# Kernel tuning notes

Measured on AMD Instinct MI355X. Metric: run time of the kernel, lower is better.

## Reference

```python
import jax, jax.numpy as jnp
import numpy as np

B, CLEN, QLEN, H = 32, 384, 64, 768


def _p(key, shape, scale=0.02):
    return jax.random.normal(key, shape, dtype=jnp.float32) * scale


def setup_inputs() -> dict:
    key = jax.random.key(0)
    ks = iter(jax.random.split(key, 64))
    d = {}
    d["c"] = jax.random.normal(next(ks), (B, CLEN, H), jnp.float32)
    d["q"] = jax.random.normal(next(ks), (B, QLEN, H), jnp.float32)
    d["w_att_c"] = _p(next(ks), (H,)); d["b_att_c"] = jnp.zeros((), jnp.float32)
    d["w_att_q"] = _p(next(ks), (H,)); d["b_att_q"] = jnp.zeros((), jnp.float32)
    d["w_att_cq"] = _p(next(ks), (H,)); d["b_att_cq"] = jnp.zeros((), jnp.float32)
    def add_lstm(prefix, in_dim):
        for dr in ("f", "b"):
            d[prefix + dr + "_wih"] = _p(next(ks), (4 * H, in_dim))
            d[prefix + dr + "_whh"] = _p(next(ks), (4 * H, H))
            d[prefix + dr + "_b"] = jnp.zeros((4 * H,), jnp.float32)  # b_ih + b_hh fused
    add_lstm("l1", 4 * H)  # modeling_LSTM1: input 4H
    add_lstm("l2", 2 * H)  # modeling_LSTM2: input 2H
    add_lstm("lo", 2 * H)  # output_LSTM: input 2H
    d["p1_wg"] = _p(next(ks), (4 * H,)); d["p1_bg"] = jnp.zeros((), jnp.float32)
    d["p1_wm"] = _p(next(ks), (2 * H,)); d["p1_bm"] = jnp.zeros((), jnp.float32)
    d["p2_wg"] = _p(next(ks), (4 * H,)); d["p2_bg"] = jnp.zeros((), jnp.float32)
    d["p2_wm"] = _p(next(ks), (2 * H,)); d["p2_bm"] = jnp.zeros((), jnp.float32)
    return d


def _lstm_dir(x, wih, whh, b):
    # single-direction LSTM, torch gate order (i, f, g, o)
    Bb, T, _ = x.shape
    Hh = whh.shape[1]
    xg = jnp.einsum("bti,gi->btg", x, wih) + b  # precompute input projections [B,T,4H]
    def step(carry, xt):
        h, cst = carry
        g = xt + h @ whh.T
        i, f, gg, o = jnp.split(g, 4, axis=-1)
        i = jax.nn.sigmoid(i); f = jax.nn.sigmoid(f)
        gg = jnp.tanh(gg); o = jax.nn.sigmoid(o)
        cst = f * cst + i * gg
        h = o * jnp.tanh(cst)
        return (h, cst), h
    init = (jnp.zeros((Bb, Hh), x.dtype), jnp.zeros((Bb, Hh), x.dtype))
    _, hs = jax.lax.scan(step, init, jnp.swapaxes(xg, 0, 1))
    return jnp.swapaxes(hs, 0, 1)


def _bilstm(x, fwih, fwhh, fb, bwih, bwhh, bb):
    hf = _lstm_dir(x, fwih, fwhh, fb)
    hb = _lstm_dir(x[:, ::-1], bwih, bwhh, bb)[:, ::-1]
    return jnp.concatenate([hf, hb], axis=-1)


def _forward(c, q,
             w_att_c, b_att_c, w_att_q, b_att_q, w_att_cq, b_att_cq,
             l1f_wih, l1f_whh, l1f_b, l1b_wih, l1b_whh, l1b_b,
             l2f_wih, l2f_whh, l2f_b, l2b_wih, l2b_whh, l2b_b,
             lof_wih, lof_whh, lof_b, lob_wih, lob_whh, lob_b,
             p1_wg, p1_bg, p1_wm, p1_bm, p2_wg, p2_bg, p2_wm, p2_bm):
    # --- att_flow_layer: trilinear similarity collapsed to a single einsum ---
    # original loops over q_len applying att_weight_cq(c * q_i); equivalent to:
    cq = jnp.einsum("bih,bjh,h->bij", c, q, w_att_cq) + b_att_cq  # [B,C,Q]
    s = (c @ w_att_c + b_att_c)[:, :, None] + (q @ w_att_q + b_att_q)[:, None, :] + cq
    a = jax.nn.softmax(s, axis=2)                       # attend context->query
    c2q = jnp.einsum("bij,bjh->bih", a, q)              # [B,C,H]
    b_w = jax.nn.softmax(jnp.max(s, axis=2), axis=1)    # [B,C]
    q2c = jnp.einsum("bi,bih->bh", b_w, c)[:, None, :]  # [B,1,H]
    g = jnp.concatenate([c, c2q, c * c2q, c * q2c], axis=-1)  # [B,C,8H? no, 4H]

    # --- modeling layers (two stacked biLSTMs) ---
    m1 = _bilstm(g, l1f_wih, l1f_whh, l1f_b, l1b_wih, l1b_whh, l1b_b)
    m = _bilstm(m1, l2f_wih, l2f_whh, l2f_b, l2b_wih, l2b_whh, l2b_b)

    # --- output layer ---
    p1 = (g @ p1_wg + p1_bg) + (m @ p1_wm + p1_bm)      # [B,C]
    m2 = _bilstm(m, lof_wih, lof_whh, lof_b, lob_wih, lob_whh, lob_b)
    p2 = (g @ p2_wg + p2_bg) + (m2 @ p2_wm + p2_bm)
    return p1, p2


def reference(c, q,
              w_att_c, b_att_c, w_att_q, b_att_q, w_att_cq, b_att_cq,
              l1f_wih, l1f_whh, l1f_b, l1b_wih, l1b_whh, l1b_b,
              l2f_wih, l2f_whh, l2f_b, l2b_wih, l2b_whh, l2b_b,
              lof_wih, lof_whh, lof_b, lob_wih, lob_whh, lob_b,
              p1_wg, p1_bg, p1_wm, p1_bm, p2_wg, p2_bg, p2_wm, p2_bm):
    return _forward(c, q,
                    w_att_c, b_att_c, w_att_q, b_att_q, w_att_cq, b_att_cq,
                    l1f_wih, l1f_whh, l1f_b, l1b_wih, l1b_whh, l1b_b,
                    l2f_wih, l2f_whh, l2f_b, l2b_wih, l2b_whh, l2b_b,
                    lof_wih, lof_whh, lof_b, lob_wih, lob_whh, lob_b,
                    p1_wg, p1_bg, p1_wm, p1_bm, p2_wg, p2_bg, p2_wm, p2_bm)
```

## Files before the change

### kernel.cpp

```cpp
#include <hip/hip_runtime.h>


typedef __bf16 bf16_t;
typedef __bf16 bf16x4 __attribute__((ext_vector_type(4)));
typedef __bf16 bf16x8 __attribute__((ext_vector_type(8)));
typedef float  f32x4  __attribute__((ext_vector_type(4)));
typedef unsigned long long ull;

#define TT 384

__device__ __forceinline__ void gload_lds16(const void* g, void* l) {
  __builtin_amdgcn_global_load_lds((const __attribute__((address_space(1))) void*)g,
                                   (__attribute__((address_space(3))) void*)l, 16, 0, 0);
}

__global__ void k_zeroE(unsigned* p) {
  int i = blockIdx.x * 256 + threadIdx.x;
  __hip_atomic_store(p + i, 0xFFFF0000u, __ATOMIC_RELAXED, __HIP_MEMORY_SCOPE_AGENT);
}

template<int BN, int EPI, int BSRC>
__global__ __launch_bounds__(256) void k_gemm(
    const bf16_t* __restrict__ A, const void* __restrict__ Bv, const void* __restrict__ Bv2,
    int nsplit, void* __restrict__ Cv,
    int M, int N, int K, long sAb, long sBb, long sCb,
    const float* __restrict__ rowb, const float* __restrict__ colb,
    const float* __restrict__ sb)
{
  constexpr int BM = 128, BK = 32;
  constexpr int NT = BN / 32;
  __shared__ bf16_t sA[BM * BK];
  __shared__ bf16_t sB[BN * BK];
  const int t    = threadIdx.x;
  const int lane = t & 63;
  const int wm   = (t >> 6) >> 1, wn = (t >> 6) & 1;
  const long bz  = blockIdx.z;
  const int nbase = blockIdx.y * BN;
  const bf16_t* Ab = A + bz * sAb + (long)blockIdx.x * BM * K;
  const bf16_t* Bb = nullptr;
  const float*  Bf = nullptr;
  if constexpr (BSRC == 0)
    Bb = (const bf16_t*)Bv + bz * sBb + (long)nbase * K;
  else
    Bf = (nbase < nsplit) ? ((const float*)Bv  + (long)nbase * K)
                          : ((const float*)Bv2 + (long)(nbase - nsplit) * K);

  const int r4 = t >> 2;
  const int kq = (t & 3) ^ ((r4 >> 1) & 3);

  f32x4 acc[4][NT];
  #pragma unroll
  for (int i = 0; i < 4; i++)
    #pragma unroll
    for (int j = 0; j < NT; j++) acc[i][j] = (f32x4){0.f, 0.f, 0.f, 0.f};

  const int mrow = lane & 15;
  const int fq   = lane >> 4;
  const int aswz = (fq ^ ((mrow >> 1) & 3)) * 8;

  for (int k0 = 0; k0 < K; k0 += BK) {
    __syncthreads();
    gload_lds16(Ab + (long)r4 * K + k0 + kq * 8,        (char*)sA + t * 16);
    gload_lds16(Ab + (long)(64 + r4) * K + k0 + kq * 8, (char*)sA + 4096 + t * 16);
    if constexpr (BSRC == 0) {
      gload_lds16(Bb + (long)r4 * K + k0 + kq * 8,        (char*)sB + t * 16);
      if constexpr (BN == 128)
        gload_lds16(Bb + (long)(64 + r4) * K + k0 + kq * 8, (char*)sB + 4096 + t * 16);
    } else {
      {
        f32x4 b0 = *(const f32x4*)(Bf + (long)r4 * K + k0 + kq * 8);
        f32x4 b1 = *(const f32x4*)(Bf + (long)r4 * K + k0 + kq * 8 + 4);
        bf16x8 bb;
        #pragma unroll
        for (int e = 0; e < 4; e++) { bb[e] = (bf16_t)b0[e]; bb[e + 4] = (bf16_t)b1[e]; }
        *(bf16x8*)((char*)sB + t * 16) = bb;
      }
      if constexpr (BN == 128) {
        f32x4 b0 = *(const f32x4*)(Bf + (long)(64 + r4) * K + k0 + kq * 8);
        f32x4 b1 = *(const f32x4*)(Bf + (long)(64 + r4) * K + k0 + kq * 8 + 4);
        bf16x8 bb;
        #pragma unroll
        for (int e = 0; e < 4; e++) { bb[e] = (bf16_t)b0[e]; bb[e + 4] = (bf16_t)b1[e]; }
        *(bf16x8*)((char*)sB + 4096 + t * 16) = bb;
      }
    }
    __syncthreads();

    bf16x8 af[4], bv[NT];
    #pragma unroll
    for (int mt = 0; mt < 4; mt++)
      af[mt] = *(const bf16x8*)(sA + (wm * 64 + mt * 16 + mrow) * 32 + aswz);
    #pragma unroll
    for (int nt = 0; nt < NT; nt++)
      bv[nt] = *(const bf16x8*)(sB + (wn * (BN / 2) + nt * 16 + mrow) * 32 + aswz);
    #pragma unroll
    for (int mt = 0; mt < 4; mt++)
      #pragma unroll
      for (int nt = 0; nt < NT; nt++)
        acc[mt][nt] = __builtin_amdgcn_mfma_f32_16x16x32_bf16(af[mt], bv[nt], acc[mt][nt], 0, 0, 0);
  }

  const int rbase = (lane >> 4) * 4;
  #pragma unroll
  for (int mt = 0; mt < 4; mt++)
    #pragma unroll
    for (int nt = 0; nt < NT; nt++)
      #pragma unroll
      for (int r = 0; r < 4; r++) {
        int grow = blockIdx.x * BM + wm * 64 + mt * 16 + rbase + r;
        int gcol = nbase + wn * (BN / 2) + nt * 16 + (lane & 15);
        if constexpr (EPI == 0) {
          ((bf16_t*)Cv)[bz * sCb + (long)grow * N + gcol] = (bf16_t)acc[mt][nt][r];
        } else {
          ((float*)Cv)[bz * sCb + (long)grow * N + gcol] =
              acc[mt][nt][r] + rowb[bz * M + grow] + colb[bz * N + gcol] + sb[0];
        }
      }
}

__global__ __launch_bounds__(256) void k_lstm(
    const bf16_t* __restrict__ xg, bf16_t* __restrict__ mout,
    unsigned* __restrict__ E,
    const float* __restrict__ whh_f, const float* __restrict__ whh_b,
    const float* __restrict__ bias_f, const float* __restrict__ bias_b,
    int tagbase)
{
  __shared__ bf16_t sW[64 * 776];
  __shared__ bf16_t sH[16 * 776];
  __shared__ float  sG[4 * 256];
  const int t    = threadIdx.x;
  const int lane = t & 63;
  const int wg   = t >> 6;
  const int blk  = blockIdx.x;
  const int dir  = blk / 96;
  const int qq   = blk - dir * 96;
  const int sl   = qq >> 1;
  const int bg   = qq & 1;
  const int j0   = sl * 16;
  const float* whh  = dir ? whh_b : whh_f;
  const float* bias = dir ? bias_b : bias_f;

  for (int r = 0; r < 64; r++) {
    if (t < 192) {
      const float* src = whh + (long)((r >> 4) * 768 + j0 + (r & 15)) * 768 + t * 4;
      f32x4 v = *(const f32x4*)src;
      bf16x4 o; o[0] = (bf16_t)v[0]; o[1] = (bf16_t)v[1]; o[2] = (bf16_t)v[2]; o[3] = (bf16_t)v[3];
      *(bf16x4*)(sW + r * 776 + t * 4) = o;
    }
  }
  const int b16 = t >> 4;
  const int jj  = t & 15;
  float bsv[4];
  #pragma unroll
  for (int gi = 0; gi < 4; gi++) bsv[gi] = bias[gi * 768 + j0 + jj];

  int soff[24];
  #pragma unroll
  for (int i = 0; i < 24; i++) {
    int e = i * 256 + t;
    soff[i] = (e / 384) * 1552 + (e % 384) * 4;
  }

  float cst = 0.f;
  const int mrow  = lane & 15;
  const int fq    = lane >> 4;
  const int boff  = (wg * 16 + mrow) * 776 + fq * 8;
  const int aoff0 = mrow * 776 + fq * 8;
  const long xrow0 = (long)(bg * 16 + b16) * TT;

  for (int s = 0; s < TT; s++) {
    const int tc = dir ? (TT - 1 - s) : s;

    float xv[4];
    {
      long xr = (xrow0 + tc) * 6144 + dir * 3072 + j0 + jj;
      #pragma unroll
      for (int gi = 0; gi < 4; gi++) xv[gi] = (float)xg[xr + gi * 768];
    }

    if (s == 0) {
      for (int e = t; e < 1552; e += 256)
        *(f32x4*)((char*)sH + e * 16) = (f32x4){0.f, 0.f, 0.f, 0.f};
    } else {
      const unsigned want = (unsigned)(tagbase + s - 1);
      const int par = (s - 1) & 1;
      const ull* src = (const ull*)E + ((long)(par * 2 + dir) * 32 + bg * 16) * 384;
      ull qv[24];
      #pragma unroll
      for (int i = 0; i < 24; i++)
        qv[i] = __hip_atomic_load(src + i * 256 + t, __ATOMIC_RELAXED, __HIP_MEMORY_SCOPE_AGENT);
      for (;;) {
        unsigned bad = 0;
        #pragma unroll
        for (int i = 0; i < 24; i++) {
          unsigned lo = (unsigned)qv[i], hi = (unsigned)(qv[i] >> 32);
          if ((lo >> 16) != want || (hi >> 16) != want) bad |= 1u << i;
        }
        if (!bad) break;
        #pragma unroll
        for (int i = 0; i < 24; i++)
          if (bad & (1u << i))
            qv[i] = __hip_atomic_load(src + i * 256 + t, __ATOMIC_RELAXED, __HIP_MEMORY_SCOPE_AGENT);
      }
      #pragma unroll
      for (int i = 0; i < 24; i++) {
        ushort2 hh;
        hh.x = (unsigned short)qv[i];
        hh.y = (unsigned short)(qv[i] >> 32);
        *(ushort2*)((char*)sH + soff[i]) = hh;
      }
    }
    __syncthreads();

    f32x4 a0 = (f32x4){0.f, 0.f, 0.f, 0.f};
    #pragma unroll
    for (int kc = 0; kc < 24; kc++) {
      bf16x8 bv = *(const bf16x8*)(sW + boff + kc * 32);
      bf16x8 av = *(const bf16x8*)(sH + aoff0 + kc * 32);
      a0 = __builtin_amdgcn_mfma_f32_16x16x32_bf16(av, bv, a0, 0, 0, 0);
    }
    #pragma unroll
    for (int r = 0; r < 4; r++)
      sG[wg * 256 + (fq * 4 + r) * 16 + mrow] = a0[r];
    __syncthreads();

    {
      float gi = sG[0 * 256 + t] + xv[0] + bsv[0];
      float gf = sG[1 * 256 + t] + xv[1] + bsv[1];
      float gg = sG[2 * 256 + t] + xv[2] + bsv[2];
      float go = sG[3 * 256 + t] + xv[3] + bsv[3];
      gi = 1.f / (1.f + __expf(-gi));
      gf = 1.f / (1.f + __expf(-gf));
      gg = 1.f - 2.f / (__expf(2.f * gg) + 1.f);
      go = 1.f / (1.f + __expf(-go));
      cst = gf * cst + gi * gg;
      float hv = go * (1.f - 2.f / (__expf(2.f * cst) + 1.f));
      union { bf16_t b; unsigned short u; } pk;
      pk.b = (bf16_t)hv;
      unsigned tag = (unsigned)(tagbase + s);
      long ed = ((long)((s & 1) * 2 + dir) * 32 + bg * 16 + b16) * 768 + j0 + jj;
      __hip_atomic_store(E + ed, (tag << 16) | pk.u,
                         __ATOMIC_RELAXED, __HIP_MEMORY_SCOPE_AGENT);
      mout[(xrow0 + tc) * 1536 + dir * 768 + j0 + jj] = pk.b;
    }
  }
}


__global__ __launch_bounds__(256) void k_pack(
    const float* __restrict__ c, const float* __restrict__ q,
    const float* __restrict__ wcq, bf16_t* __restrict__ cw, bf16_t* __restrict__ qb)
{
  int i = blockIdx.x * 256 + threadIdx.x;
  if (i < 9437184) {
    int h = i % 768;
    cw[i] = (bf16_t)(c[i] * wcq[h]);
  } else {
    int j = i - 9437184;
    qb[j] = (bf16_t)q[j];
  }
}

__global__ __launch_bounds__(256) void k_proj(
    const float* __restrict__ c, const float* __restrict__ q,
    const float* __restrict__ wc, const float* __restrict__ bc,
    const float* __restrict__ wq, const float* __restrict__ bq,
    float* __restrict__ projc, float* __restrict__ projq)
{
  int row  = blockIdx.x * 4 + (threadIdx.x >> 6);
  int lane = threadIdx.x & 63;
  const float *src, *w;
  bool isC = row < 12288;
  if (isC) { src = c + (long)row * 768;          w = wc; }
  else     { src = q + (long)(row - 12288) * 768; w = wq; }
  float a = 0.f;
  for (int k = lane * 4; k < 768; k += 256) {
    f32x4 v = *(const f32x4*)(src + k);
    f32x4 wv = *(const f32x4*)(w + k);
    a += v[0]*wv[0] + v[1]*wv[1] + v[2]*wv[2] + v[3]*wv[3];
  }
  for (int m = 32; m; m >>= 1) a += __shfl_xor(a, m);
  if (lane == 0) {
    if (isC) projc[row] = a + bc[0];
    else     projq[row - 12288] = a + bq[0];
  }
}

__global__ __launch_bounds__(256) void k_smax_j(
    const float* __restrict__ s, bf16_t* __restrict__ a, float* __restrict__ smax)
{
  int row  = blockIdx.x * 4 + (threadIdx.x >> 6);
  int lane = threadIdx.x & 63;
  float v = s[(long)row * 64 + lane];
  float mx = v;
  for (int m = 32; m; m >>= 1) mx = fmaxf(mx, __shfl_xor(mx, m));
  float p = __expf(v - mx);
  float sum = p;
  for (int m = 32; m; m >>= 1) sum += __shfl_xor(sum, m);
  a[(long)row * 64 + lane] = (bf16_t)(p / sum);
  if (lane == 0) smax[row] = mx;
}

__global__ __launch_bounds__(384) void k_smax_i(
    const float* __restrict__ smax, float* __restrict__ bw)
{
  __shared__ float red[8];
  int b = blockIdx.x, t = threadIdx.x;
  int lane = t & 63, wv = t >> 6;
  float v = smax[b * 384 + t];
  float mx = v;
  for (int m = 32; m; m >>= 1) mx = fmaxf(mx, __shfl_xor(mx, m));
  if (lane == 0) red[wv] = mx;
  __syncthreads();
  float gm = red[0];
  #pragma unroll
  for (int i = 1; i < 6; i++) gm = fmaxf(gm, red[i]);
  float p = __expf(v - gm);
  float sm = p;
  for (int m = 32; m; m >>= 1) sm += __shfl_xor(sm, m);
  __syncthreads();
  if (lane == 0) red[wv] = sm;
  __syncthreads();
  float tot = red[0];
  #pragma unroll
  for (int i = 1; i < 6; i++) tot += red[i];
  bw[b * 384 + t] = p / tot;
}

__global__ __launch_bounds__(256) void k_q2c(
    const float* __restrict__ bw, const float* __restrict__ c, float* __restrict__ q2c)
{
  int b = blockIdx.y;
  int h = blockIdx.x * 256 + threadIdx.x;
  const float* cb = c + (long)b * 384 * 768;
  float acc = 0.f;
  for (int i = 0; i < 384; i++) acc += bw[b * 384 + i] * cb[(long)i * 768 + h];
  q2c[b * 768 + h] = acc;
}

__global__ __launch_bounds__(256) void k_tq(
    const bf16_t* __restrict__ qb, bf16_t* __restrict__ qT)
{
  __shared__ bf16_t sT[64][72];
  int b = blockIdx.y, hc = blockIdx.x, t = threadIdx.x;
  {
    int j = t >> 2, h0 = (t & 3) * 16;
    const bf16_t* src = qb + (long)(b * 64 + j) * 768 + hc * 64 + h0;
    *(bf16x8*)&sT[j][h0]     = *(const bf16x8*)(src);
    *(bf16x8*)&sT[j][h0 + 8] = *(const bf16x8*)(src + 8);
  }
  __syncthreads();
  {
    int h = t >> 2, j0 = (t & 3) * 16;
    bf16x8 o0, o1;
    #pragma unroll
    for (int e = 0; e < 8; e++) { o0[e] = sT[j0 + e][h]; o1[e] = sT[j0 + 8 + e][h]; }
    bf16_t* dst = qT + (long)(b * 768 + hc * 64 + h) * 64 + j0;
    *(bf16x8*)dst       = o0;
    *(bf16x8*)(dst + 8) = o1;
  }
}

__global__ __launch_bounds__(256) void k_buildg(
    const float* __restrict__ c, const bf16_t* __restrict__ c2q,
    const float* __restrict__ q2c, bf16_t* __restrict__ g)
{
  int i = blockIdx.x * 256 + threadIdx.x;
  int h = i % 768;
  int row = i / 768;
  int b = row / 384;
  float cv  = c[i];
  float cqv = (float)c2q[i];
  float qcv = q2c[b * 768 + h];
  bf16_t* gr = g + (long)row * 3072;
  gr[h]        = (bf16_t)cv;
  gr[768 + h]  = c2q[i];
  gr[1536 + h] = (bf16_t)(cv * cqv);
  gr[2304 + h] = (bf16_t)(cv * qcv);
}

__global__ __launch_bounds__(256) void k_headsg(
    const bf16_t* __restrict__ g, const float* __restrict__ w1, const float* __restrict__ w2,
    float* __restrict__ pg1, float* __restrict__ pg2)
{
  int row  = blockIdx.x * 4 + (threadIdx.x >> 6);
  int lane = threadIdx.x & 63;
  float a1 = 0.f, a2 = 0.f;
  const bf16_t* gr = g + (long)row * 3072;
  for (int k = lane * 8; k < 3072; k += 512) {
    bf16x8 v = *(const bf16x8*)(gr + k);
    f32x4 wa = *(const f32x4*)(w1 + k), wb = *(const f32x4*)(w1 + k + 4);
    f32x4 xa = *(const f32x4*)(w2 + k), xb = *(const f32x4*)(w2 + k + 4);
    #pragma unroll
    for (int e = 0; e < 4; e++) {
      a1 += (float)v[e] * wa[e] + (float)v[e + 4] * wb[e];
      a2 += (float)v[e] * xa[e] + (float)v[e + 4] * xb[e];
    }
  }
  for (int m_ = 32; m_; m_ >>= 1) { a1 += __shfl_xor(a1, m_); a2 += __shfl_xor(a2, m_); }
  if (lane == 0) { pg1[row] = a1; pg2[row] = a2; }
}

__global__ __launch_bounds__(256) void k_headsm(
    const bf16_t* __restrict__ m, const float* __restrict__ wm,
    const float* __restrict__ pg, const float* __restrict__ bg,
    const float* __restrict__ bm, float* __restrict__ out)
{
  int row  = blockIdx.x * 4 + (threadIdx.x >> 6);
  int lane = threadIdx.x & 63;
  float a = 0.f;
  const bf16_t* mr = m + (long)row * 1536;
  for (int k = lane * 8; k < 1536; k += 512) {
    bf16x8 v = *(const bf16x8*)(mr + k);
    f32x4 wa = *(const f32x4*)(wm + k), wb = *(const f32x4*)(wm + k + 4);
    #pragma unroll
    for (int e = 0; e < 4; e++) a += (float)v[e] * wa[e] + (float)v[e + 4] * wb[e];
  }
  for (int m_ = 32; m_; m_ >>= 1) a += __shfl_xor(a, m_);
  if (lane == 0) out[row] = pg[row] + a + bg[0] + bm[0];
}


extern "C" void kernel_launch(void* const* d_in, const int* in_sizes, int n_in,
                              void* d_out, int out_size, void* d_ws, size_t ws_size,
                              hipStream_t stream)
{
  (void)in_sizes; (void)n_in; (void)out_size; (void)ws_size;
  const float* c    = (const float*)d_in[0];
  const float* q    = (const float*)d_in[1];
  const float* wac  = (const float*)d_in[2];
  const float* bac  = (const float*)d_in[3];
  const float* waq  = (const float*)d_in[4];
  const float* baq  = (const float*)d_in[5];
  const float* wacq = (const float*)d_in[6];
  const float* bacq = (const float*)d_in[7];
  const float* l1f_wih = (const float*)d_in[8];
  const float* l1f_whh = (const float*)d_in[9];
  const float* l1f_b   = (const float*)d_in[10];
  const float* l1b_wih = (const float*)d_in[11];
  const float* l1b_whh = (const float*)d_in[12];
  const float* l1b_b   = (const float*)d_in[13];
  const float* l2f_wih = (const float*)d_in[14];
  const float* l2f_whh = (const float*)d_in[15];
  const float* l2f_b   = (const float*)d_in[16];
  const float* l2b_wih = (const float*)d_in[17];
  const float* l2b_whh = (const float*)d_in[18];
  const float* l2b_b   = (const float*)d_in[19];
  const float* lof_wih = (const float*)d_in[20];
  const float* lof_whh = (const float*)d_in[21];
  const float* lof_b   = (const float*)d_in[22];
  const float* lob_wih = (const float*)d_in[23];
  const float* lob_whh = (const float*)d_in[24];
  const float* lob_b   = (const float*)d_in[25];
  const float* p1wg = (const float*)d_in[26];
  const float* p1bg = (const float*)d_in[27];
  const float* p1wm = (const float*)d_in[28];
  const float* p1bm = (const float*)d_in[29];
  const float* p2wg = (const float*)d_in[30];
  const float* p2bg = (const float*)d_in[31];
  const float* p2wm = (const float*)d_in[32];
  const float* p2bm = (const float*)d_in[33];

  char* ws = (char*)d_ws;
  bf16_t* g_bf = (bf16_t*)ws;
  bf16_t* mA   = (bf16_t*)ws;
  bf16_t* mB   = (bf16_t*)(ws + 37748736L);
  bf16_t* m2   = (bf16_t*)ws;
  char*   xgc  = ws + 75497472L;
  bf16_t* xg   = (bf16_t*)xgc;
  bf16_t* cw  = (bf16_t*)xgc;
  bf16_t* qb  = (bf16_t*)(xgc + 18874368L);
  bf16_t* qT  = (bf16_t*)(xgc + 22020096L);
  float*  sS  = (float*) (xgc + 25165824L);
  bf16_t* aP  = (bf16_t*)(xgc + 28311552L);
  bf16_t* c2q = (bf16_t*)(xgc + 29884416L);
  char* tail = ws + 226492416L;
  float*    projc = (float*)tail;
  float*    projq = (float*)(tail + 49152);
  float*    smax  = (float*)(tail + 57344);
  float*    bw    = (float*)(tail + 106496);
  float*    q2c   = (float*)(tail + 155648);
  float*    pg1   = (float*)(tail + 253952);
  float*    pg2   = (float*)(tail + 303104);
  unsigned* E     = (unsigned*)(tail + 352256);

  k_zeroE<<<768, 256, 0, stream>>>(E);

  k_pack<<<43008, 256, 0, stream>>>(c, q, wacq, cw, qb);
  k_proj<<<3584, 256, 0, stream>>>(c, q, wac, bac, waq, baq, projc, projq);
  k_gemm<64,1,0><<<dim3(3,1,32), 256, 0, stream>>>(cw, qb, nullptr, 1<<30, sS,
      384, 64, 768, (long)384*768, (long)64*768, (long)384*64, projc, projq, bacq);
  k_smax_j<<<3072, 256, 0, stream>>>(sS, aP, smax);
  k_smax_i<<<32, 384, 0, stream>>>(smax, bw);
  k_q2c<<<dim3(3,32), 256, 0, stream>>>(bw, c, q2c);
  k_tq<<<dim3(12,32), 256, 0, stream>>>(qb, qT);
  k_gemm<64,0,0><<<dim3(3,12,32), 256, 0, stream>>>(aP, qT, nullptr, 1<<30, c2q,
      384, 768, 64, (long)384*64, (long)768*64, (long)384*768, nullptr, nullptr, nullptr);
  k_buildg<<<36864, 256, 0, stream>>>(c, c2q, q2c, g_bf);
  k_headsg<<<3072, 256, 0, stream>>>(g_bf, p1wg, p2wg, pg1, pg2);

  k_gemm<128,0,1><<<dim3(96,48,1), 256, 0, stream>>>(g_bf, l1f_wih, l1b_wih, 3072, xg,
      12288, 6144, 3072, 0, 0, 0, nullptr, nullptr, nullptr);
  k_lstm<<<192, 256, 0, stream>>>(xg, mA, E, l1f_whh, l1b_whh, l1f_b, l1b_b, 0);

  k_gemm<128,0,1><<<dim3(96,48,1), 256, 0, stream>>>(mA, l2f_wih, l2b_wih, 3072, xg,
      12288, 6144, 1536, 0, 0, 0, nullptr, nullptr, nullptr);
  k_lstm<<<192, 256, 0, stream>>>(xg, mB, E, l2f_whh, l2b_whh, l2f_b, l2b_b, 384);
  k_headsm<<<3072, 256, 0, stream>>>(mB, p1wm, pg1, p1bg, p1bm, (float*)d_out);

  k_gemm<128,0,1><<<dim3(96,48,1), 256, 0, stream>>>(mB, lof_wih, lob_wih, 3072, xg,
      12288, 6144, 1536, 0, 0, 0, nullptr, nullptr, nullptr);
  k_lstm<<<192, 256, 0, stream>>>(xg, m2, E, lof_whh, lob_whh, lof_b, lob_b, 768);
  k_headsm<<<3072, 256, 0, stream>>>(m2, p2wm, pg2, p2bg, p2bm, (float*)d_out + 12288);
}
```

Measured before the change: 6.965 ms.

## Hold recurrent LSTM weights in registers, halve block count with 512-thread blocks

The persistent LSTM kernel now keeps each wave's slice of W_hh in VGPRs as bf16 fragments instead of in LDS, and each block covers 32 hidden units with 8 waves instead of 16 units with 4 waves. The grid drops from 192 to 96 blocks, so fewer blocks take part in the per-step global flag synchronisation and each block polls half as much of the exchange buffer per thread. The MFMA loop is split into two independent accumulators, and the gate scratch in LDS is padded to avoid bank conflicts. In exchange, each block does twice the matrix work per step with fewer CUs active, and 24 bf16x8 weight registers per thread increase register pressure.

Result: faster. 6.563 ms (-5.8%).

```diff
diff --git a/kernel.cpp b/kernel.cpp
--- a/kernel.cpp
+++ b/kernel.cpp
@@ -118,53 +118,60 @@
       }
 }
 
-__global__ __launch_bounds__(256) void k_lstm(
+__global__ __launch_bounds__(512) void k_lstm(
     const bf16_t* __restrict__ xg, bf16_t* __restrict__ mout,
     unsigned* __restrict__ E,
     const float* __restrict__ whh_f, const float* __restrict__ whh_b,
     const float* __restrict__ bias_f, const float* __restrict__ bias_b,
     int tagbase)
 {
-  __shared__ bf16_t sW[64 * 776];
   __shared__ bf16_t sH[16 * 776];
-  __shared__ float  sG[4 * 256];
+  __shared__ float  sG[4 * 544];
   const int t    = threadIdx.x;
   const int lane = t & 63;
-  const int wg   = t >> 6;
+  const int w    = t >> 6;
+  const int g    = w & 3;
+  const int ch   = w >> 2;
   const int blk  = blockIdx.x;
-  const int dir  = blk / 96;
-  const int qq   = blk - dir * 96;
+  const int dir  = blk / 48;
+  const int qq   = blk - dir * 48;
   const int sl   = qq >> 1;
   const int bg   = qq & 1;
-  const int j0   = sl * 16;
+  const int j0   = sl * 32;
   const float* whh  = dir ? whh_b : whh_f;
   const float* bias = dir ? bias_b : bias_f;
 
-  for (int r = 0; r < 64; r++) {
-    if (t < 192) {
-      const float* src = whh + (long)((r >> 4) * 768 + j0 + (r & 15)) * 768 + t * 4;
-      f32x4 v = *(const f32x4*)src;
-      bf16x4 o; o[0] = (bf16_t)v[0]; o[1] = (bf16_t)v[1]; o[2] = (bf16_t)v[2]; o[3] = (bf16_t)v[3];
-      *(bf16x4*)(sW + r * 776 + t * 4) = o;
-    }
-  }
-  const int b16 = t >> 4;
-  const int jj  = t & 15;
+  const int mrow = lane & 15;
+  const int fq   = lane >> 4;
+
+  bf16x8 bw[24];
+  {
+    const float* wrow = whh + (long)(g * 768 + j0 + ch * 16 + mrow) * 768 + fq * 8;
+    #pragma unroll
+    for (int kc = 0; kc < 24; kc++) {
+      f32x4 v0 = *(const f32x4*)(wrow + kc * 32);
+      f32x4 v1 = *(const f32x4*)(wrow + kc * 32 + 4);
+      bf16x8 bb;
+      #pragma unroll
+      for (int e = 0; e < 4; e++) { bb[e] = (bf16_t)v0[e]; bb[e + 4] = (bf16_t)v1[e]; }
+      bw[kc] = bb;
+    }
+  }
+
+  const int b16 = t >> 5;
+  const int jj  = t & 31;
   float bsv[4];
   #pragma unroll
   for (int gi = 0; gi < 4; gi++) bsv[gi] = bias[gi * 768 + j0 + jj];
 
-  int soff[24];
+  int soff[12];
   #pragma unroll
-  for (int i = 0; i < 24; i++) {
-    int e = i * 256 + t;
+  for (int i = 0; i < 12; i++) {
+    int e = i * 512 + t;
     soff[i] = (e / 384) * 1552 + (e % 384) * 4;
   }
 
   float cst = 0.f;
-  const int mrow  = lane & 15;
-  const int fq    = lane >> 4;
-  const int boff  = (wg * 16 + mrow) * 776 + fq * 8;
   const int aoff0 = mrow * 776 + fq * 8;
   const long xrow0 = (long)(bg * 16 + b16) * TT;
 
@@ -179,31 +186,31 @@
     }
 
     if (s == 0) {
-      for (int e = t; e < 1552; e += 256)
+      for (int e = t; e < 1552; e += 512)
         *(f32x4*)((char*)sH + e * 16) = (f32x4){0.f, 0.f, 0.f, 0.f};
     } else {
       const unsigned want = (unsigned)(tagbase + s - 1);
       const int par = (s - 1) & 1;
       const ull* src = (const ull*)E + ((long)(par * 2 + dir) * 32 + bg * 16) * 384;
-      ull qv[24];
+      ull qv[12];
       #pragma unroll
-      for (int i = 0; i < 24; i++)
-        qv[i] = __hip_atomic_load(src + i * 256 + t, __ATOMIC_RELAXED, __HIP_MEMORY_SCOPE_AGENT);
+      for (int i = 0; i < 12; i++)
+        qv[i] = __hip_atomic_load(src + i * 512 + t, __ATOMIC_RELAXED, __HIP_MEMORY_SCOPE_AGENT);
       for (;;) {
         unsigned bad = 0;
         #pragma unroll
-        for (int i = 0; i < 24; i++) {
+        for (int i = 0; i < 12; i++) {
           unsigned lo = (unsigned)qv[i], hi = (unsigned)(qv[i] >> 32);
           if ((lo >> 16) != want || (hi >> 16) != want) bad |= 1u << i;
         }
         if (!bad) break;
         #pragma unroll
-        for (int i = 0; i < 24; i++)
+        for (int i = 0; i < 12; i++)
           if (bad & (1u << i))
-            qv[i] = __hip_atomic_load(src + i * 256 + t, __ATOMIC_RELAXED, __HIP_MEMORY_SCOPE_AGENT);
+            qv[i] = __hip_atomic_load(src + i * 512 + t, __ATOMIC_RELAXED, __HIP_MEMORY_SCOPE_AGENT);
       }
       #pragma unroll
-      for (int i = 0; i < 24; i++) {
+      for (int i = 0; i < 12; i++) {
         ushort2 hh;
         hh.x = (unsigned short)qv[i];
         hh.y = (unsigned short)(qv[i] >> 32);
@@ -213,22 +220,24 @@
     __syncthreads();
 
     f32x4 a0 = (f32x4){0.f, 0.f, 0.f, 0.f};
-    #pragma unroll
-    for (int kc = 0; kc < 24; kc++) {
-      bf16x8 bv = *(const bf16x8*)(sW + boff + kc * 32);
-      bf16x8 av = *(const bf16x8*)(sH + aoff0 + kc * 32);
-      a0 = __builtin_amdgcn_mfma_f32_16x16x32_bf16(av, bv, a0, 0, 0, 0);
+    f32x4 a1 = (f32x4){0.f, 0.f, 0.f, 0.f};
+    #pragma unroll
+    for (int kc = 0; kc < 24; kc += 2) {
+      bf16x8 av0 = *(const bf16x8*)(sH + aoff0 + kc * 32);
+      bf16x8 av1 = *(const bf16x8*)(sH + aoff0 + kc * 32 + 32);
+      a0 = __builtin_amdgcn_mfma_f32_16x16x32_bf16(av0, bw[kc],     a0, 0, 0, 0);
+      a1 = __builtin_amdgcn_mfma_f32_16x16x32_bf16(av1, bw[kc + 1], a1, 0, 0, 0);
     }
     #pragma unroll
     for (int r = 0; r < 4; r++)
-      sG[wg * 256 + (fq * 4 + r) * 16 + mrow] = a0[r];
+      sG[g * 544 + (ch * 16 + mrow) * 17 + fq * 4 + r] = a0[r] + a1[r];
     __syncthreads();
 
     {
-      float gi = sG[0 * 256 + t] + xv[0] + bsv[0];
-      float gf = sG[1 * 256 + t] + xv[1] + bsv[1];
-      float gg = sG[2 * 256 + t] + xv[2] + bsv[2];
-      float go = sG[3 * 256 + t] + xv[3] + bsv[3];
+      float gi = sG[0 * 544 + jj * 17 + b16] + xv[0] + bsv[0];
+      float gf = sG[1 * 544 + jj * 17 + b16] + xv[1] + bsv[1];
+      float gg = sG[2 * 544 + jj * 17 + b16] + xv[2] + bsv[2];
+      float go = sG[3 * 544 + jj * 17 + b16] + xv[3] + bsv[3];
       gi = 1.f / (1.f + __expf(-gi));
       gf = 1.f / (1.f + __expf(-gf));
       gg = 1.f - 2.f / (__expf(2.f * gg) + 1.f);
@@ -501,15 +510,15 @@
 
   k_gemm<128,0,1><<<dim3(96,48,1), 256, 0, stream>>>(g_bf, l1f_wih, l1b_wih, 3072, xg,
       12288, 6144, 3072, 0, 0, 0, nullptr, nullptr, nullptr);
-  k_lstm<<<192, 256, 0, stream>>>(xg, mA, E, l1f_whh, l1b_whh, l1f_b, l1b_b, 0);
+  k_lstm<<<96, 512, 0, stream>>>(xg, mA, E, l1f_whh, l1b_whh, l1f_b, l1b_b, 0);
 
   k_gemm<128,0,1><<<dim3(96,48,1), 256, 0, stream>>>(mA, l2f_wih, l2b_wih, 3072, xg,
       12288, 6144, 1536, 0, 0, 0, nullptr, nullptr, nullptr);
-  k_lstm<<<192, 256, 0, stream>>>(xg, mB, E, l2f_whh, l2b_whh, l2f_b, l2b_b, 384);
+  k_lstm<<<96, 512, 0, stream>>>(xg, mB, E, l2f_whh, l2b_whh, l2f_b, l2b_b, 384);
   k_headsm<<<3072, 256, 0, stream>>>(mB, p1wm, pg1, p1bg, p1bm, (float*)d_out);
 
   k_gemm<128,0,1><<<dim3(96,48,1), 256, 0, stream>>>(mB, lof_wih, lob_wih, 3072, xg,
       12288, 6144, 1536, 0, 0, 0, nullptr, nullptr, nullptr);
-  k_lstm<<<192, 256, 0, stream>>>(xg, m2, E, lof_whh, lob_whh, lof_b, lob_b, 768);
+  k_lstm<<<96, 512, 0, stream>>>(xg, m2, E, lof_whh, lob_whh, lof_b, lob_b, 768);
   k_headsm<<<3072, 256, 0, stream>>>(m2, p2wm, pg2, p2bg, p2bm, (float*)d_out + 12288);
 }
```
